# Performance work log

Hardware: AMD Instinct MI355X
Metric: run time of the kernel (lower is better)

## Reference

```python
import jax, jax.numpy as jnp
import numpy as np

T, B, I, H = 512, 64, 1024, 1024


def setup_inputs() -> dict:
    key = jax.random.key(0)
    ks = jax.random.split(key, 16)
    d = {
        "inputs": jax.random.normal(ks[0], (T, B, I), dtype=jnp.float32),
        "hx": jnp.zeros((B, H), dtype=jnp.float32),
        "cx": jnp.zeros((B, H), dtype=jnp.float32),
        # weights [H, I] / [H, H] as in nn.Parameter(torch.randn(...)); scaled down for stability
        "w_ii": jax.random.normal(ks[1], (H, I), jnp.float32) * 0.02,
        "w_fi": jax.random.normal(ks[2], (H, I), jnp.float32) * 0.02,
        "w_ai": jax.random.normal(ks[3], (H, I), jnp.float32) * 0.02,
        "w_oi": jax.random.normal(ks[4], (H, I), jnp.float32) * 0.02,
        "w_ih": jax.random.normal(ks[5], (H, H), jnp.float32) * 0.02,
        "w_fh": jax.random.normal(ks[6], (H, H), jnp.float32) * 0.02,
        "w_ah": jax.random.normal(ks[7], (H, H), jnp.float32) * 0.02,
        "w_oh": jax.random.normal(ks[8], (H, H), jnp.float32) * 0.02,
        "b_i": jax.random.uniform(ks[9], (H,), jnp.float32),
        "b_f": jax.random.uniform(ks[10], (H,), jnp.float32),
        "b_a": jax.random.uniform(ks[11], (H,), jnp.float32),
        "b_o": jax.random.normal(ks[12], (H,), jnp.float32),
    }
    return d


def reference(inputs, hx, cx, w_ii, w_fi, w_ai, w_oi, w_ih, w_fh, w_ah, w_oh,
              b_i, b_f, b_a, b_o):
    # FP quant type -> weight proxies and quant activations are identity;
    # layer_norm='identity'; rec_quant/out_quant are IdentityQuant.
    # Stack the 4 gate matrices so each step does one [B,I]x[I,4H] and one
    # [B,H]x[H,4H] GEMM (same math as the 8 separate torch.mm calls).
    Wi = jnp.concatenate([w_ii, w_fi, w_ai, w_oi], axis=0).T  # [I, 4H]
    Wh = jnp.concatenate([w_ih, w_fh, w_ah, w_oh], axis=0).T  # [H, 4H]
    b = jnp.concatenate([b_i, b_f, b_a, b_o], axis=0)          # [4H]
    Hh = hx.shape[-1]

    def step(carry, x_t):
        h, c = carry
        gates = x_t @ Wi + h @ Wh + b                 # [B, 4H]
        i_g, f_g, a_g, o_g = jnp.split(gates, 4, axis=-1)
        i_g = jax.nn.sigmoid(i_g)
        f_g = jax.nn.sigmoid(f_g)
        a_g = jnp.tanh(a_g)
        o_g = jax.nn.sigmoid(o_g)
        cy = f_g * c + i_g * a_g
        hy = o_g * jnp.tanh(cy)
        return (hy, cy), hy

    (hy, cy), outputs = jax.lax.scan(step, (hx, cx), inputs)
    return outputs, hy, cy
```

## Files before the change

### kernel.cpp

```cpp
#include <hip/hip_runtime.h>
#include <cstdint>

typedef _Float16 half8 __attribute__((ext_vector_type(8)));
typedef _Float16 half4v __attribute__((ext_vector_type(4)));
typedef float floatx4 __attribute__((ext_vector_type(4)));
typedef unsigned long long u64;

__device__ __forceinline__ float sig_(float x) { return 1.f / (1.f + __expf(-x)); }
__device__ __forceinline__ float tanh_(float x) {
  x = fminf(15.f, fmaxf(-15.f, x));
  float e = __expf(2.f * x);
  return (e - 1.f) / (e + 1.f);
}

__global__ void cvt_x_kernel(const float* __restrict__ x, _Float16* __restrict__ xh, int n) {
  int i = (blockIdx.x * 256 + threadIdx.x) * 4;
  if (i < n) {
    const float4 v = *(const float4*)(x + i);
    half4v o = {(_Float16)v.x, (_Float16)v.y, (_Float16)v.z, (_Float16)v.w};
    *(half4v*)(xh + i) = o;
  }
}

__global__ void build_w_kernel(const float* w0, const float* w1, const float* w2, const float* w3,
                               const float* w4, const float* w5, const float* w6, const float* w7,
                               const float* b0, const float* b1, const float* b2, const float* b3,
                               _Float16* __restrict__ Wip, _Float16* __restrict__ Whp,
                               float* __restrict__ biasp) {
  int n = blockIdx.x;
  if (n < 8192) {
    const float* srcs[8] = {w0, w1, w2, w3, w4, w5, w6, w7};
    int which = n >> 12;
    int row = n & 4095;
    int u = row >> 2, g = row & 3;
    const float* s = srcs[which * 4 + g] + (size_t)u * 1024;
    _Float16* dst = (which ? Whp : Wip) + (size_t)row * 1024;
    int t = threadIdx.x * 4;
    float4 v = *(const float4*)(s + t);
    half4v o = {(_Float16)v.x, (_Float16)v.y, (_Float16)v.z, (_Float16)v.w};
    *(half4v*)(dst + t) = o;
  } else {
    const float* bs[4] = {b0, b1, b2, b3};
    for (int idx = threadIdx.x; idx < 4096; idx += 256)
      biasp[idx] = bs[idx & 3][idx >> 2];
  }
}

__global__ void init_h_kernel(const float* __restrict__ hx, unsigned int* __restrict__ hbuf) {
  int i = blockIdx.x * 256 + threadIdx.x;
  if (i < 32768) {
    unsigned short lo = __builtin_bit_cast(unsigned short, (_Float16)hx[2 * i]);
    unsigned short hi = __builtin_bit_cast(unsigned short, (_Float16)hx[2 * i + 1]);
    hbuf[i] = (unsigned int)lo | ((unsigned int)hi << 16);
  }
}

__global__ void zero_flags_kernel(unsigned int* __restrict__ flags) {
  int i = blockIdx.x * 256 + threadIdx.x;
  if (i < 8192) flags[i] = 0u;
}

__global__ __launch_bounds__(256) void gemm_g_kernel(const _Float16* __restrict__ Xh,
                                                     const _Float16* __restrict__ Wp,
                                                     const float* __restrict__ biasp,
                                                     _Float16* __restrict__ G3) {
  __shared__ _Float16 Al[4][128][8];
  __shared__ _Float16 Bl[4][128][8];
  const int tid = threadIdx.x;
  const int w = tid >> 6, l = tid & 63;
  const int wm = (w >> 1) * 64, wn = (w & 1) * 64;
  const int ml = l & 15, kg = l >> 4;
  const int bm = blockIdx.x, bn = blockIdx.y;
  const int r0 = tid & 127, kc0 = tid >> 7;
  const int kc1 = kc0 + 2;
  const size_t arow0 = (size_t)(bm * 128 + r0) * 1024;
  const size_t brow0 = (size_t)(bn * 128 + r0) * 1024;
  floatx4 acc[4][4] = {};
  for (int kt = 0; kt < 1024; kt += 32) {
    __syncthreads();
    __builtin_amdgcn_global_load_lds(
        (const __attribute__((address_space(1))) unsigned int*)(Xh + arow0 + kt + kc0 * 8),
        (__attribute__((address_space(3))) unsigned int*)&Al[kc0][r0][0], 16, 0, 0);
    __builtin_amdgcn_global_load_lds(
        (const __attribute__((address_space(1))) unsigned int*)(Xh + arow0 + kt + kc1 * 8),
        (__attribute__((address_space(3))) unsigned int*)&Al[kc1][r0][0], 16, 0, 0);
    __builtin_amdgcn_global_load_lds(
        (const __attribute__((address_space(1))) unsigned int*)(Wp + brow0 + kt + kc0 * 8),
        (__attribute__((address_space(3))) unsigned int*)&Bl[kc0][r0][0], 16, 0, 0);
    __builtin_amdgcn_global_load_lds(
        (const __attribute__((address_space(1))) unsigned int*)(Wp + brow0 + kt + kc1 * 8),
        (__attribute__((address_space(3))) unsigned int*)&Bl[kc1][r0][0], 16, 0, 0);
    __syncthreads();
    half8 af[4], bf[4];
#pragma unroll
    for (int i = 0; i < 4; ++i) af[i] = *(const half8*)&Al[kg][wm + i * 16 + ml][0];
#pragma unroll
    for (int j = 0; j < 4; ++j) bf[j] = *(const half8*)&Bl[kg][wn + j * 16 + ml][0];
#pragma unroll
    for (int i = 0; i < 4; ++i)
#pragma unroll
      for (int j = 0; j < 4; ++j)
        acc[i][j] = __builtin_amdgcn_mfma_f32_16x16x32_f16(af[i], bf[j], acc[i][j], 0, 0, 0);
  }
  const int t = (bm * 128 + wm) >> 6;
#pragma unroll
  for (int j = 0; j < 4; ++j) {
    const int col = bn * 128 + wn + j * 16 + ml;
    const float bj = biasp[col];
    const int p = col >> 4;
#pragma unroll
    for (int i = 0; i < 4; ++i) {
      half4v pk = {(_Float16)(acc[i][j][0] + bj), (_Float16)(acc[i][j][1] + bj),
                   (_Float16)(acc[i][j][2] + bj), (_Float16)(acc[i][j][3] + bj)};
      *(half4v*)&G3[((size_t)p * 512 + t) * 1024 + i * 256 + kg * 64 + ml * 4] = pk;
    }
  }
}

__global__ __launch_bounds__(256, 1) void lstm_rec_kernel(
    const _Float16* __restrict__ G3, const _Float16* __restrict__ Whp,
    unsigned int* __restrict__ hbuf, const float* __restrict__ cx,
    float* __restrict__ out, unsigned int* __restrict__ flags) {
  const int p = blockIdx.x, tid = threadIdx.x;
  const int w = tid >> 6, l = tid & 63;
  const int ml = l & 15, kg = l >> 4;
  __shared__ _Float16 hl_[32768];
  char* hl = (char*)(hl_ + w * 8192);

  half8 wfr[32];
#pragma unroll
  for (int s = 0; s < 32; ++s)
    wfr[s] = *(const half8*)&Whp[(size_t)(16 * p + ml) * 1024 + s * 32 + kg * 8];

  const int bl = l >> 2, u = l & 3;
  const int bglob = 16 * w + bl, U = 4 * p + u;
  float c = cx[bglob * 1024 + U];
  __syncthreads();

  for (int t = 0; t < 512; ++t) {
    const u64* hq = (const u64*)(hbuf + (size_t)(t & 1) * 32768);
    u64* hnq = (u64*)(hbuf + (size_t)((t & 1) ^ 1) * 32768);

    u64 c1[32], c2[32];
#pragma unroll
    for (int i = 0; i < 32; ++i) {
      const int row = i >> 1, j = ((i & 1) << 6) + l;
      c1[i] = __hip_atomic_load(&hq[(size_t)(16 * w + row) * 256 + j], __ATOMIC_RELAXED,
                                __HIP_MEMORY_SCOPE_AGENT);
    }
    const u64 ginb =
        *(const u64*)&G3[((size_t)p * 512 + t) * 1024 + w * 256 + kg * 64 + ml * 4];
#pragma unroll
    for (int i = 0; i < 32; ++i) {
      const int row = i >> 1, j = ((i & 1) << 6) + l;
      c2[i] = __hip_atomic_load(&hq[(size_t)(16 * w + row) * 256 + 128 + j], __ATOMIC_RELAXED,
                                __HIP_MEMORY_SCOPE_AGENT);
    }

#pragma unroll
    for (int i = 0; i < 32; ++i) {
      const int row = i >> 1, j = ((i & 1) << 6) + l;
      const int un = (j >> 1) ^ (row & 7);
      *(u64*)(hl + row * 1024 + un * 16 + (j & 1) * 8) = c1[i];
    }
    __builtin_amdgcn_wave_barrier();
    floatx4 acc[4] = {};
#pragma unroll
    for (int s = 0; s < 16; ++s) {
      const int un = (s * 4 + kg) ^ (ml & 7);
      half8 a = *(const half8*)(hl + ml * 1024 + un * 16);
      acc[s & 3] = __builtin_amdgcn_mfma_f32_16x16x32_f16(a, wfr[s], acc[s & 3], 0, 0, 0);
    }
    __builtin_amdgcn_wave_barrier();
#pragma unroll
    for (int i = 0; i < 32; ++i) {
      const int row = i >> 1, j = ((i & 1) << 6) + l;
      const int un = (j >> 1) ^ (row & 7);
      *(u64*)(hl + row * 1024 + un * 16 + (j & 1) * 8) = c2[i];
    }
    __builtin_amdgcn_wave_barrier();
#pragma unroll
    for (int s = 0; s < 16; ++s) {
      const int un = (s * 4 + kg) ^ (ml & 7);
      half8 a = *(const half8*)(hl + ml * 1024 + un * 16);
      acc[s & 3] = __builtin_amdgcn_mfma_f32_16x16x32_f16(a, wfr[16 + s], acc[s & 3], 0, 0, 0);
    }
    floatx4 a4 = (acc[0] + acc[1]) + (acc[2] + acc[3]);

    union { u64 q; half4v h4; } gu; gu.q = ginb;
    float* glw = (float*)hl;
    __builtin_amdgcn_wave_barrier();
#pragma unroll
    for (int r = 0; r < 4; ++r)
      glw[(kg * 4 + r) * 20 + ml] = a4[r] + (float)gu.h4[r];
    __builtin_amdgcn_wave_barrier();
    const float4 g4 = *(const float4*)&glw[bl * 20 + u * 4];

    const float ig = sig_(g4.x), fg = sig_(g4.y);
    const float ag = tanh_(g4.z), og = sig_(g4.w);
    c = fg * c + ig * ag;
    const float h = og * tanh_(c);

    unsigned int mine = (unsigned int)__builtin_bit_cast(unsigned short, (_Float16)h);
    unsigned int pair = mine | (((unsigned int)__shfl_xor((int)mine, 1)) << 16);
    u64 quad = (u64)pair | ((u64)(unsigned int)__shfl_xor((int)pair, 2) << 32);
    if (u == 0)
      __hip_atomic_store(&hnq[(size_t)bglob * 256 + p], quad, __ATOMIC_RELAXED,
                         __HIP_MEMORY_SCOPE_AGENT);

    if (t == 511) {
      out[(size_t)t * 65536 + bglob * 1024 + U] = h;
      out[(size_t)33554432 + bglob * 1024 + U] = h;
      out[(size_t)33619968 + bglob * 1024 + U] = c;
      break;
    }

    __builtin_amdgcn_s_waitcnt(0x0F70);
    __syncthreads();
    if (tid == 0)
      __hip_atomic_store(&flags[p * 32], (unsigned)(t + 1), __ATOMIC_RELAXED,
                         __HIP_MEMORY_SCOPE_AGENT);
    out[(size_t)t * 65536 + bglob * 1024 + U] = h;
    const unsigned tgt = (unsigned)(t + 1);
    int done;
    do {
      unsigned v = __hip_atomic_load(&flags[tid * 32], __ATOMIC_RELAXED,
                                     __HIP_MEMORY_SCOPE_AGENT);
      done = __syncthreads_and((int)(v >= tgt));
      if (!done) __builtin_amdgcn_s_sleep(2);
    } while (!done);
    asm volatile("" ::: "memory");
  }
}

extern "C" void kernel_launch(void* const* d_in, const int* in_sizes, int n_in,
                              void* d_out, int out_size, void* d_ws, size_t ws_size,
                              hipStream_t stream) {
  const float* x    = (const float*)d_in[0];
  const float* hx   = (const float*)d_in[1];
  const float* cxp  = (const float*)d_in[2];
  const float* w_ii = (const float*)d_in[3];
  const float* w_fi = (const float*)d_in[4];
  const float* w_ai = (const float*)d_in[5];
  const float* w_oi = (const float*)d_in[6];
  const float* w_ih = (const float*)d_in[7];
  const float* w_fh = (const float*)d_in[8];
  const float* w_ah = (const float*)d_in[9];
  const float* w_oh = (const float*)d_in[10];
  const float* b_i  = (const float*)d_in[11];
  const float* b_f  = (const float*)d_in[12];
  const float* b_a  = (const float*)d_in[13];
  const float* b_o  = (const float*)d_in[14];
  float* out = (float*)d_out;

  char* ws = (char*)d_ws;
  _Float16* Xh        = (_Float16*)(ws);
  unsigned int* flags = (unsigned int*)(ws);
  _Float16* Wip       = (_Float16*)(ws + 67108864);
  _Float16* Whp       = (_Float16*)(ws + 75497472);
  float* biasp        = (float*)(ws + 83886080);
  unsigned int* hbuf  = (unsigned int*)(ws + 83902464);
  _Float16* G3        = (_Float16*)(ws + 84164864);
  if (ws_size < (size_t)84164864 + 268435456) return;

  cvt_x_kernel<<<32768, 256, 0, stream>>>(x, Xh, 33554432);
  build_w_kernel<<<8193, 256, 0, stream>>>(w_ii, w_fi, w_ai, w_oi, w_ih, w_fh, w_ah, w_oh,
                                           b_i, b_f, b_a, b_o, Wip, Whp, biasp);
  init_h_kernel<<<128, 256, 0, stream>>>(hx, hbuf);
  gemm_g_kernel<<<dim3(256, 32), 256, 0, stream>>>(Xh, Wip, biasp, G3);
  zero_flags_kernel<<<32, 256, 0, stream>>>(flags);
  lstm_rec_kernel<<<256, 256, 0, stream>>>(G3, Whp, hbuf, cxp, out, flags);
}
```

Before: 3.799 ms.

## Halve persistent recurrent blocks, share h tile in LDS, single-wave flag polling

The persistent LSTM recurrence now runs as 128 blocks of 512 threads instead of 256 blocks of 256, each block owning 8 hidden units across two column groups. The h tile for a step is loaded once per block into shared LDS and read by all eight waves, rather than each wave staging its own copy. The grid barrier now has one wave poll packed 64-bit flags with no sleep, then release the other waves through an LDS token. The intent is to cut global h traffic and the number of blocks in the cross-block barrier, at the cost of block-wide __syncthreads inside each step and busy-spinning waves.

```diff
diff --git a/kernel.cpp b/kernel.cpp
--- a/kernel.cpp
+++ b/kernel.cpp
@@ -117,79 +117,86 @@
   }
 }
 
-__global__ __launch_bounds__(256, 1) void lstm_rec_kernel(
+__global__ __launch_bounds__(512, 2) void lstm_rec_kernel(
     const _Float16* __restrict__ G3, const _Float16* __restrict__ Whp,
     unsigned int* __restrict__ hbuf, const float* __restrict__ cx,
     float* __restrict__ out, unsigned int* __restrict__ flags) {
   const int p = blockIdx.x, tid = threadIdx.x;
   const int w = tid >> 6, l = tid & 63;
+  const int bg = w & 3, cg = w >> 2;
   const int ml = l & 15, kg = l >> 4;
-  __shared__ _Float16 hl_[32768];
-  char* hl = (char*)(hl_ + w * 8192);
+  __shared__ __align__(16) char lds[141328];
 
   half8 wfr[32];
+  const size_t wrow = (size_t)(32 * p + 16 * cg + ml) * 1024;
 #pragma unroll
   for (int s = 0; s < 32; ++s)
-    wfr[s] = *(const half8*)&Whp[(size_t)(16 * p + ml) * 1024 + s * 32 + kg * 8];
+    wfr[s] = *(const half8*)&Whp[wrow + s * 32 + kg * 8];
 
   const int bl = l >> 2, u = l & 3;
-  const int bglob = 16 * w + bl, U = 4 * p + u;
-  float c = cx[bglob * 1024 + U];
+  const int batch = 16 * bg + bl;
+  const int U = 8 * p + 4 * cg + u;
+  float c = cx[batch * 1024 + U];
+
+  const int tq = tid >> 7;
+  const int j0 = tid & 127;
+  unsigned* tok = (unsigned*)(lds + 141312);
+  if (tid == 0) *tok = 0u;
+  float* glw = (float*)(lds + 131072) + w * 320;
   __syncthreads();
 
   for (int t = 0; t < 512; ++t) {
-    const u64* hq = (const u64*)(hbuf + (size_t)(t & 1) * 32768);
-    u64* hnq = (u64*)(hbuf + (size_t)((t & 1) ^ 1) * 32768);
-
-    u64 c1[32], c2[32];
-#pragma unroll
-    for (int i = 0; i < 32; ++i) {
-      const int row = i >> 1, j = ((i & 1) << 6) + l;
-      c1[i] = __hip_atomic_load(&hq[(size_t)(16 * w + row) * 256 + j], __ATOMIC_RELAXED,
+    const u64* hq = (const u64*)hbuf + (size_t)(t & 1) * 16384;
+    u64* hnq = (u64*)hbuf + (size_t)((t & 1) ^ 1) * 16384;
+
+    u64 c1[16], c2[16];
+#pragma unroll
+    for (int i = 0; i < 16; ++i) {
+      const int rg = i * 4 + tq;
+      c1[i] = __hip_atomic_load(&hq[(size_t)rg * 256 + j0], __ATOMIC_RELAXED,
                                 __HIP_MEMORY_SCOPE_AGENT);
     }
-    const u64 ginb =
-        *(const u64*)&G3[((size_t)p * 512 + t) * 1024 + w * 256 + kg * 64 + ml * 4];
-#pragma unroll
-    for (int i = 0; i < 32; ++i) {
-      const int row = i >> 1, j = ((i & 1) << 6) + l;
-      c2[i] = __hip_atomic_load(&hq[(size_t)(16 * w + row) * 256 + 128 + j], __ATOMIC_RELAXED,
+    const u64 ginb = *(const u64*)&G3[((size_t)(2 * p + cg) * 512 + t) * 1024 +
+                                      bg * 256 + kg * 64 + ml * 4];
+#pragma unroll
+    for (int i = 0; i < 16; ++i) {
+      const int rg = i * 4 + tq;
+      c2[i] = __hip_atomic_load(&hq[(size_t)rg * 256 + 128 + j0], __ATOMIC_RELAXED,
                                 __HIP_MEMORY_SCOPE_AGENT);
     }
 
 #pragma unroll
-    for (int i = 0; i < 32; ++i) {
-      const int row = i >> 1, j = ((i & 1) << 6) + l;
-      const int un = (j >> 1) ^ (row & 7);
-      *(u64*)(hl + row * 1024 + un * 16 + (j & 1) * 8) = c1[i];
-    }
-    __builtin_amdgcn_wave_barrier();
+    for (int i = 0; i < 16; ++i) {
+      const int rg = i * 4 + tq, bgr = rg >> 4, row = rg & 15;
+      const int un = (j0 >> 1) ^ (row & 7);
+      *(u64*)(lds + bgr * 16384 + row * 1024 + un * 16 + (j0 & 1) * 8) = c1[i];
+    }
+    __syncthreads();
     floatx4 acc[4] = {};
+    const char* sl0 = lds + bg * 16384 + ml * 1024;
 #pragma unroll
     for (int s = 0; s < 16; ++s) {
       const int un = (s * 4 + kg) ^ (ml & 7);
-      half8 a = *(const half8*)(hl + ml * 1024 + un * 16);
+      half8 a = *(const half8*)(sl0 + un * 16);
       acc[s & 3] = __builtin_amdgcn_mfma_f32_16x16x32_f16(a, wfr[s], acc[s & 3], 0, 0, 0);
     }
-    __builtin_amdgcn_wave_barrier();
-#pragma unroll
-    for (int i = 0; i < 32; ++i) {
-      const int row = i >> 1, j = ((i & 1) << 6) + l;
-      const int un = (j >> 1) ^ (row & 7);
-      *(u64*)(hl + row * 1024 + un * 16 + (j & 1) * 8) = c2[i];
-    }
-    __builtin_amdgcn_wave_barrier();
+#pragma unroll
+    for (int i = 0; i < 16; ++i) {
+      const int rg = i * 4 + tq, bgr = rg >> 4, row = rg & 15;
+      const int un = (j0 >> 1) ^ (row & 7);
+      *(u64*)(lds + (4 + bgr) * 16384 + row * 1024 + un * 16 + (j0 & 1) * 8) = c2[i];
+    }
+    __syncthreads();
+    const char* sl1 = lds + (4 + bg) * 16384 + ml * 1024;
 #pragma unroll
     for (int s = 0; s < 16; ++s) {
       const int un = (s * 4 + kg) ^ (ml & 7);
-      half8 a = *(const half8*)(hl + ml * 1024 + un * 16);
+      half8 a = *(const half8*)(sl1 + un * 16);
       acc[s & 3] = __builtin_amdgcn_mfma_f32_16x16x32_f16(a, wfr[16 + s], acc[s & 3], 0, 0, 0);
     }
     floatx4 a4 = (acc[0] + acc[1]) + (acc[2] + acc[3]);
 
     union { u64 q; half4v h4; } gu; gu.q = ginb;
-    float* glw = (float*)hl;
-    __builtin_amdgcn_wave_barrier();
 #pragma unroll
     for (int r = 0; r < 4; ++r)
       glw[(kg * 4 + r) * 20 + ml] = a4[r] + (float)gu.h4[r];
@@ -205,30 +212,33 @@
     unsigned int pair = mine | (((unsigned int)__shfl_xor((int)mine, 1)) << 16);
     u64 quad = (u64)pair | ((u64)(unsigned int)__shfl_xor((int)pair, 2) << 32);
     if (u == 0)
-      __hip_atomic_store(&hnq[(size_t)bglob * 256 + p], quad, __ATOMIC_RELAXED,
+      __hip_atomic_store(&hnq[(size_t)batch * 256 + 2 * p + cg], quad, __ATOMIC_RELAXED,
                          __HIP_MEMORY_SCOPE_AGENT);
 
     if (t == 511) {
-      out[(size_t)t * 65536 + bglob * 1024 + U] = h;
-      out[(size_t)33554432 + bglob * 1024 + U] = h;
-      out[(size_t)33619968 + bglob * 1024 + U] = c;
+      out[(size_t)t * 65536 + batch * 1024 + U] = h;
+      out[(size_t)33554432 + batch * 1024 + U] = h;
+      out[(size_t)33619968 + batch * 1024 + U] = c;
       break;
     }
 
     __builtin_amdgcn_s_waitcnt(0x0F70);
     __syncthreads();
+    const unsigned tgt = (unsigned)(t + 1);
     if (tid == 0)
-      __hip_atomic_store(&flags[p * 32], (unsigned)(t + 1), __ATOMIC_RELAXED,
-                         __HIP_MEMORY_SCOPE_AGENT);
-    out[(size_t)t * 65536 + bglob * 1024 + U] = h;
-    const unsigned tgt = (unsigned)(t + 1);
-    int done;
-    do {
-      unsigned v = __hip_atomic_load(&flags[tid * 32], __ATOMIC_RELAXED,
-                                     __HIP_MEMORY_SCOPE_AGENT);
-      done = __syncthreads_and((int)(v >= tgt));
-      if (!done) __builtin_amdgcn_s_sleep(2);
-    } while (!done);
+      __hip_atomic_store(&flags[p], tgt, __ATOMIC_RELAXED, __HIP_MEMORY_SCOPE_AGENT);
+    out[(size_t)t * 65536 + batch * 1024 + U] = h;
+    if (w == 0) {
+      const u64* f64 = (const u64*)flags;
+      int done;
+      do {
+        u64 v = __hip_atomic_load(&f64[l], __ATOMIC_RELAXED, __HIP_MEMORY_SCOPE_AGENT);
+        done = __all(((unsigned)v >= tgt) & ((unsigned)(v >> 32) >= tgt));
+      } while (!done);
+      __hip_atomic_store(tok, tgt, __ATOMIC_RELAXED, __HIP_MEMORY_SCOPE_WORKGROUP);
+    } else {
+      while (__hip_atomic_load(tok, __ATOMIC_RELAXED, __HIP_MEMORY_SCOPE_WORKGROUP) < tgt) {}
+    }
     asm volatile("" ::: "memory");
   }
 }
@@ -269,5 +279,5 @@
   init_h_kernel<<<128, 256, 0, stream>>>(hx, hbuf);
   gemm_g_kernel<<<dim3(256, 32), 256, 0, stream>>>(Xh, Wip, biasp, G3);
   zero_flags_kernel<<<32, 256, 0, stream>>>(flags);
-  lstm_rec_kernel<<<256, 256, 0, stream>>>(G3, Whp, hbuf, cxp, out, flags);
-}
+  lstm_rec_kernel<<<128, 512, 0, stream>>>(G3, Whp, hbuf, cxp, out, flags);
+}
```

After: 4.764 ms. 25.4% more time.

## Split recurrent GEMM across waves by K and reduce partial sums in LDS

Applied to the files above, without the earlier changes.

Each block now owns 16 batch rows by 64 hidden-unit columns, and its four waves split the K dimension rather than the batch. Every lane loads only its own h fragment straight into registers, which removes the LDS staging, the swizzled shared-memory writes and the per-step global h traffic of 64 rows per block. Partial accumulators from the four waves are written to LDS and summed after a block barrier before the gate nonlinearities. This shrinks per-step load volume and latency on the serial critical path, at the cost of an extra __syncthreads and an LDS reduction each step.

```diff
diff --git a/kernel.cpp b/kernel.cpp
--- a/kernel.cpp
+++ b/kernel.cpp
@@ -121,106 +121,93 @@
     const _Float16* __restrict__ G3, const _Float16* __restrict__ Whp,
     unsigned int* __restrict__ hbuf, const float* __restrict__ cx,
     float* __restrict__ out, unsigned int* __restrict__ flags) {
-  const int p = blockIdx.x, tid = threadIdx.x;
-  const int w = tid >> 6, l = tid & 63;
+  const int P = blockIdx.x, tid = threadIdx.x;
+  const int kw = tid >> 6, l = tid & 63;
   const int ml = l & 15, kg = l >> 4;
-  __shared__ _Float16 hl_[32768];
-  char* hl = (char*)(hl_ + w * 8192);
+  const int bg = P >> 6, ug = P & 63;
+  __shared__ float pacc[4][16][68];
 
   half8 wfr[32];
 #pragma unroll
-  for (int s = 0; s < 32; ++s)
-    wfr[s] = *(const half8*)&Whp[(size_t)(16 * p + ml) * 1024 + s * 32 + kg * 8];
-
-  const int bl = l >> 2, u = l & 3;
-  const int bglob = 16 * w + bl, U = 4 * p + u;
-  float c = cx[bglob * 1024 + U];
+  for (int cgt = 0; cgt < 4; ++cgt)
+#pragma unroll
+    for (int s = 0; s < 8; ++s)
+      wfr[cgt * 8 + s] =
+          *(const half8*)&Whp[(size_t)(64 * ug + 16 * cgt + ml) * 1024 + (8 * kw + s) * 32 + kg * 8];
+
+  const int b16 = tid >> 4, u16 = tid & 15;
+  const int batch = 16 * bg + b16, U = 16 * ug + u16;
+  float c = cx[batch * 1024 + U];
   __syncthreads();
 
   for (int t = 0; t < 512; ++t) {
     const u64* hq = (const u64*)(hbuf + (size_t)(t & 1) * 32768);
     u64* hnq = (u64*)(hbuf + (size_t)((t & 1) ^ 1) * 32768);
 
-    u64 c1[32], c2[32];
-#pragma unroll
-    for (int i = 0; i < 32; ++i) {
-      const int row = i >> 1, j = ((i & 1) << 6) + l;
-      c1[i] = __hip_atomic_load(&hq[(size_t)(16 * w + row) * 256 + j], __ATOMIC_RELAXED,
-                                __HIP_MEMORY_SCOPE_AGENT);
-    }
-    const u64 ginb =
-        *(const u64*)&G3[((size_t)p * 512 + t) * 1024 + w * 256 + kg * 64 + ml * 4];
-#pragma unroll
-    for (int i = 0; i < 32; ++i) {
-      const int row = i >> 1, j = ((i & 1) << 6) + l;
-      c2[i] = __hip_atomic_load(&hq[(size_t)(16 * w + row) * 256 + 128 + j], __ATOMIC_RELAXED,
-                                __HIP_MEMORY_SCOPE_AGENT);
-    }
-
-#pragma unroll
-    for (int i = 0; i < 32; ++i) {
-      const int row = i >> 1, j = ((i & 1) << 6) + l;
-      const int un = (j >> 1) ^ (row & 7);
-      *(u64*)(hl + row * 1024 + un * 16 + (j & 1) * 8) = c1[i];
-    }
-    __builtin_amdgcn_wave_barrier();
+    u64 cp[16];
+#pragma unroll
+    for (int s = 0; s < 8; ++s) {
+      const size_t base = (size_t)(16 * bg + ml) * 256 + 64 * kw + 8 * s + 2 * kg;
+      cp[2 * s] = __hip_atomic_load(&hq[base], __ATOMIC_RELAXED, __HIP_MEMORY_SCOPE_AGENT);
+      cp[2 * s + 1] =
+          __hip_atomic_load(&hq[base + 1], __ATOMIC_RELAXED, __HIP_MEMORY_SCOPE_AGENT);
+    }
+    const u64 ginb = *(const u64*)&G3[(((size_t)(4 * ug + kw) * 512 + t) * 1024) +
+                                      bg * 256 + kg * 64 + ml * 4];
+
     floatx4 acc[4] = {};
 #pragma unroll
-    for (int s = 0; s < 16; ++s) {
-      const int un = (s * 4 + kg) ^ (ml & 7);
-      half8 a = *(const half8*)(hl + ml * 1024 + un * 16);
-      acc[s & 3] = __builtin_amdgcn_mfma_f32_16x16x32_f16(a, wfr[s], acc[s & 3], 0, 0, 0);
-    }
-    __builtin_amdgcn_wave_barrier();
-#pragma unroll
-    for (int i = 0; i < 32; ++i) {
-      const int row = i >> 1, j = ((i & 1) << 6) + l;
-      const int un = (j >> 1) ^ (row & 7);
-      *(u64*)(hl + row * 1024 + un * 16 + (j & 1) * 8) = c2[i];
-    }
-    __builtin_amdgcn_wave_barrier();
-#pragma unroll
-    for (int s = 0; s < 16; ++s) {
-      const int un = (s * 4 + kg) ^ (ml & 7);
-      half8 a = *(const half8*)(hl + ml * 1024 + un * 16);
-      acc[s & 3] = __builtin_amdgcn_mfma_f32_16x16x32_f16(a, wfr[16 + s], acc[s & 3], 0, 0, 0);
-    }
-    floatx4 a4 = (acc[0] + acc[1]) + (acc[2] + acc[3]);
+    for (int s = 0; s < 8; ++s) {
+      union { u64 q[2]; half8 h; } au;
+      au.q[0] = cp[2 * s];
+      au.q[1] = cp[2 * s + 1];
+#pragma unroll
+      for (int cgt = 0; cgt < 4; ++cgt)
+        acc[cgt] = __builtin_amdgcn_mfma_f32_16x16x32_f16(au.h, wfr[cgt * 8 + s], acc[cgt], 0, 0, 0);
+    }
 
     union { u64 q; half4v h4; } gu; gu.q = ginb;
-    float* glw = (float*)hl;
-    __builtin_amdgcn_wave_barrier();
-#pragma unroll
-    for (int r = 0; r < 4; ++r)
-      glw[(kg * 4 + r) * 20 + ml] = a4[r] + (float)gu.h4[r];
-    __builtin_amdgcn_wave_barrier();
-    const float4 g4 = *(const float4*)&glw[bl * 20 + u * 4];
-
-    const float ig = sig_(g4.x), fg = sig_(g4.y);
-    const float ag = tanh_(g4.z), og = sig_(g4.w);
+#pragma unroll
+    for (int cgt = 0; cgt < 4; ++cgt) {
+#pragma unroll
+      for (int r = 0; r < 4; ++r) {
+        float v = acc[cgt][r];
+        if (cgt == kw) v += (float)gu.h4[r];
+        pacc[kw][kg * 4 + r][16 * cgt + ml] = v;
+      }
+    }
+    __syncthreads();
+
+    floatx4 ssum = *(const floatx4*)&pacc[0][b16][4 * u16];
+#pragma unroll
+    for (int kw2 = 1; kw2 < 4; ++kw2)
+      ssum += *(const floatx4*)&pacc[kw2][b16][4 * u16];
+
+    const float ig = sig_(ssum[0]), fg = sig_(ssum[1]);
+    const float ag = tanh_(ssum[2]), og = sig_(ssum[3]);
     c = fg * c + ig * ag;
     const float h = og * tanh_(c);
 
     unsigned int mine = (unsigned int)__builtin_bit_cast(unsigned short, (_Float16)h);
     unsigned int pair = mine | (((unsigned int)__shfl_xor((int)mine, 1)) << 16);
     u64 quad = (u64)pair | ((u64)(unsigned int)__shfl_xor((int)pair, 2) << 32);
-    if (u == 0)
-      __hip_atomic_store(&hnq[(size_t)bglob * 256 + p], quad, __ATOMIC_RELAXED,
+    if ((u16 & 3) == 0)
+      __hip_atomic_store(&hnq[(size_t)batch * 256 + 4 * ug + (u16 >> 2)], quad,
+                         __ATOMIC_RELAXED, __HIP_MEMORY_SCOPE_AGENT);
+
+    if (t == 511) {
+      out[(size_t)t * 65536 + batch * 1024 + U] = h;
+      out[(size_t)33554432 + batch * 1024 + U] = h;
+      out[(size_t)33619968 + batch * 1024 + U] = c;
+      break;
+    }
+
+    __builtin_amdgcn_s_waitcnt(0x0F70);
+    __syncthreads();
+    if (tid == 0)
+      __hip_atomic_store(&flags[P * 32], (unsigned)(t + 1), __ATOMIC_RELAXED,
                          __HIP_MEMORY_SCOPE_AGENT);
-
-    if (t == 511) {
-      out[(size_t)t * 65536 + bglob * 1024 + U] = h;
-      out[(size_t)33554432 + bglob * 1024 + U] = h;
-      out[(size_t)33619968 + bglob * 1024 + U] = c;
-      break;
-    }
-
-    __builtin_amdgcn_s_waitcnt(0x0F70);
-    __syncthreads();
-    if (tid == 0)
-      __hip_atomic_store(&flags[p * 32], (unsigned)(t + 1), __ATOMIC_RELAXED,
-                         __HIP_MEMORY_SCOPE_AGENT);
-    out[(size_t)t * 65536 + bglob * 1024 + U] = h;
+    out[(size_t)t * 65536 + batch * 1024 + U] = h;
     const unsigned tgt = (unsigned)(t + 1);
     int done;
     do {
```

Result: faster. 3.453 ms (-9.1%).
